# Optimization experiments

Hardware: AMD Instinct MI355X
Metric: run time of the kernel (lower is better)

The kernel has to match this reference:

```python
import jax, jax.numpy as jnp
import numpy as np

N_NODES = 100000
N_EDGES = 1600000
IN_DIM, HID, OUT = 64, 128, 128
NUM_GRAPHS = 64
BN_EPS = 1e-5


def setup_inputs() -> dict:
    key = jax.random.key(0)
    ks = jax.random.split(key, 16)
    x = jax.random.normal(ks[0], (N_NODES, IN_DIM), dtype=jnp.float32)
    edge_index = jax.random.randint(ks[1], (2, N_EDGES), 0, N_NODES, dtype=jnp.int32)
    batch = jnp.sort(jax.random.randint(ks[2], (N_NODES,), 0, NUM_GRAPHS, dtype=jnp.int32))
    dims = [IN_DIM, HID, HID, OUT]
    inp = {"x": x, "edge_index": edge_index, "batch": batch}
    for i in range(3):
        din, dout = dims[i], dims[i + 1]
        s = 1.0 / np.sqrt(din)
        inp[f"Ws{i}"] = jax.random.uniform(ks[3 + 4 * i], (din, dout), jnp.float32, -s, s)
        inp[f"Wi{i}"] = jax.random.uniform(ks[4 + 4 * i], (din, dout), jnp.float32, -s, s)
        inp[f"Wo{i}"] = jax.random.uniform(ks[5 + 4 * i], (din, dout), jnp.float32, -s, s)
        inp[f"g{i}"] = jnp.ones((dout,), jnp.float32)
        inp[f"b{i}"] = jnp.zeros((dout,), jnp.float32)
    return inp


def _dgcn(x, src, dst, Ws, Wi, Wo, gamma, beta):
    # directed aggregation: in-edges (messages from src land on dst) and out-edges
    agg_in = jax.ops.segment_sum(x[src], dst, num_segments=N_NODES)   # [N, d]
    agg_out = jax.ops.segment_sum(x[dst], src, num_segments=N_NODES)  # [N, d]
    out = x @ Ws + agg_in @ Wi + agg_out @ Wo
    out = jax.nn.relu(out)
    # BatchNorm1d (training mode, biased variance, as in torch)
    mu = out.mean(axis=0)
    var = ((out - mu) ** 2).mean(axis=0)
    return gamma * (out - mu) * jax.lax.rsqrt(var + BN_EPS) + beta


def reference(x, edge_index, batch, Ws0, Wi0, Wo0, g0, b0, Ws1, Wi1, Wo1, g1, b1,
              Ws2, Wi2, Wo2, g2, b2):
    src, dst = edge_index[0], edge_index[1]
    h = _dgcn(x, src, dst, Ws0, Wi0, Wo0, g0, b0)
    h = _dgcn(h, src, dst, Ws1, Wi1, Wo1, g1, b1)
    h = _dgcn(h, src, dst, Ws2, Wi2, Wo2, g2, b2)
    # global mean pool over graphs (dropout is identity at inference)
    sums = jax.ops.segment_sum(h, batch, num_segments=NUM_GRAPHS)       # [G, OUT]
    cnts = jax.ops.segment_sum(jnp.ones((N_NODES,), h.dtype), batch, num_segments=NUM_GRAPHS)
    return sums / jnp.maximum(cnts, 1.0)[:, None]
```

## Files before the change

kernel.cpp:

```cpp
#include <hip/hip_runtime.h>

#define NN 100000
#define NE 1600000
#define NG 64
#define BN_EPS 1e-5f

#define TOT (2 * NN)
#define STB 256

#define NB 98
#define BCAP 36864
#define EPB ((NE + 1023) / 1024)

typedef __attribute__((ext_vector_type(8))) short bf16x8;
typedef __attribute__((ext_vector_type(8))) unsigned short u16x8;
typedef __attribute__((ext_vector_type(4))) float f32x4;

__device__ __forceinline__ float bf2f(unsigned short u) {
  unsigned int i = (unsigned int)u << 16;
  float f; __builtin_memcpy(&f, &i, 4); return f;
}
__device__ __forceinline__ unsigned short f2bf(float f) {
  unsigned int i; __builtin_memcpy(&i, &f, 4);
  i += 0x7FFFu + ((i >> 16) & 1u);
  return (unsigned short)(i >> 16);
}

__device__ __forceinline__ int lower_bound_dev(const int* a, int n, int key) {
  int lo = 0, hi = n;
  while (lo < hi) { int mid = (lo + hi) >> 1; if (a[mid] < key) lo = mid + 1; else hi = mid; }
  return lo;
}

__global__ __launch_bounds__(256) void k_p1(const int* __restrict__ src,
    const int* __restrict__ dst, int* __restrict__ gcur, unsigned int* __restrict__ pairs) {
  __shared__ unsigned int lbuf[NB][64];
  __shared__ int lcnt[NB], lbase[NB];
  __shared__ int sc[256];
  int t = threadIdx.x;
  if (t < NB) lcnt[t] = 0;
  __syncthreads();
  int e0 = blockIdx.x * EPB;
  int e1 = min(e0 + EPB, NE);
  for (int e = e0 + t; e < e1; e += 256) {
    int s = src[e], d = dst[e];
    {
      int key = d;
      unsigned int val = ((unsigned int)(key & 2047) << 17) | (unsigned int)s;
      int bk = key >> 11;
      int p = atomicAdd(&lcnt[bk], 1);
      if (p < 64) lbuf[bk][p] = val;
      else { int g = atomicAdd(&gcur[bk], 1); pairs[(size_t)bk * BCAP + g] = val; }
    }
    {
      int key = s + NN;
      unsigned int val = ((unsigned int)(key & 2047) << 17) | (unsigned int)d;
      int bk = key >> 11;
      int p = atomicAdd(&lcnt[bk], 1);
      if (p < 64) lbuf[bk][p] = val;
      else { int g = atomicAdd(&gcur[bk], 1); pairs[(size_t)bk * BCAP + g] = val; }
    }
  }
  __syncthreads();
  if (t < NB) {
    int c = min(lcnt[t], 64);
    lcnt[t] = c;
    lbase[t] = atomicAdd(&gcur[t], c);
  }
  __syncthreads();
  sc[t] = (t < NB) ? lcnt[t] : 0;
  __syncthreads();
  for (int off = 1; off < 256; off <<= 1) {
    int x = (t >= off) ? sc[t - off] : 0;
    __syncthreads();
    sc[t] += x;
    __syncthreads();
  }
  int total = sc[NB - 1];
  for (int idx = t; idx < total; idx += 256) {
    int lo = 0, hi = NB - 1;
    while (lo < hi) { int mid = (lo + hi) >> 1; if (sc[mid] > idx) hi = mid; else lo = mid + 1; }
    int within = idx - ((lo == 0) ? 0 : sc[lo - 1]);
    pairs[(size_t)lo * BCAP + lbase[lo] + within] = lbuf[lo][within];
  }
}

__global__ void k_scan98(const int* __restrict__ gcur, int* __restrict__ fbase) {
  __shared__ int sc[128];
  int t = threadIdx.x;
  sc[t] = (t < NB) ? gcur[t] : 0;
  __syncthreads();
  for (int off = 1; off < 128; off <<= 1) {
    int x = (t >= off) ? sc[t - off] : 0;
    __syncthreads();
    sc[t] += x;
    __syncthreads();
  }
  if (t < NB) fbase[t] = (t == 0) ? 0 : sc[t - 1];
  if (t == 0) fbase[NB] = sc[NB - 1];
}

__global__ __launch_bounds__(256) void k_p2(const unsigned int* __restrict__ pairs,
    const int* __restrict__ gcur, const int* __restrict__ fbase,
    int* __restrict__ offs, int* __restrict__ nbr) {
  int b = blockIdx.x;
  int n = gcur[b];
  int base = fbase[b];
  __shared__ int hist[2048];
  __shared__ int sc[256];
  int t = threadIdx.x;
  #pragma unroll
  for (int j = 0; j < 8; ++j) hist[t * 8 + j] = 0;
  __syncthreads();
  const unsigned int* bp = pairs + (size_t)b * BCAP;
  for (int i = t; i < n; i += 256) atomicAdd(&hist[bp[i] >> 17], 1);
  __syncthreads();
  int v[8]; int tsum = 0;
  #pragma unroll
  for (int j = 0; j < 8; ++j) { v[j] = hist[t * 8 + j]; tsum += v[j]; }
  sc[t] = tsum;
  __syncthreads();
  for (int off = 1; off < 256; off <<= 1) {
    int x = (t >= off) ? sc[t - off] : 0;
    __syncthreads();
    sc[t] += x;
    __syncthreads();
  }
  int run = (t == 0) ? 0 : sc[t - 1];
  #pragma unroll
  for (int j = 0; j < 8; ++j) {
    int key = b * 2048 + t * 8 + j;
    if (key < TOT) offs[key] = base + run;
    hist[t * 8 + j] = run;
    run += v[j];
  }
  if (b == NB - 1 && t == 0) offs[TOT] = base + n;
  __syncthreads();
  for (int i = t; i < n; i += 256) {
    unsigned int u = bp[i];
    int lk = (int)(u >> 17);
    int pos = atomicAdd(&hist[lk], 1);
    nbr[base + pos] = (int)(u & 0x1FFFFu);
  }
}

__global__ __launch_bounds__(256) void k_cvt_x(const float* __restrict__ x,
                                               unsigned short* __restrict__ xb) {
  size_t i = (size_t)blockIdx.x * 256 + threadIdx.x;
  if (i >= (size_t)NN * 16) return;
  float4 v = *(const float4*)(x + i * 4);
  ushort4 o;
  o.x = f2bf(v.x); o.y = f2bf(v.y); o.z = f2bf(v.z); o.w = f2bf(v.w);
  *(ushort4*)(xb + i * 4) = o;
}

struct WtArgs { const float* W[9]; };
__global__ __launch_bounds__(256) void k_wt(WtArgs a, unsigned short* __restrict__ wt) {
  int t = blockIdx.x * 256 + threadIdx.x;
  if (t >= 15360) return;
  int p, rem, KS;
  if (t < 3072) { p = t >> 10; rem = t & 1023; KS = 2; }
  else { int u = t - 3072; p = 3 + (u >> 11); rem = u & 2047; KS = 4; }
  int ks = rem >> 9;
  int rem2 = rem & 511;
  int nt = rem2 >> 6;
  int lane = rem2 & 63;
  int L = p / 3, op = p - L * 3;
  int lbase = (L == 0) ? 0 : (24576 + (L - 1) * 49152);
  size_t dst = (size_t)lbase + (size_t)op * KS * 4096 + (size_t)(ks * 8 + nt) * 512 + lane * 8;
  const float* W = a.W[p];
  int krow = ks * 32 + (lane >> 4) * 8;
  int col = nt * 16 + (lane & 15);
  #pragma unroll
  for (int j = 0; j < 8; ++j)
    wt[dst + j] = f2bf(W[(size_t)(krow + j) * 128 + col]);
}

__global__ void k_ssid(float* __restrict__ ss) {
  int t = threadIdx.x;
  ss[t] = 1.f; ss[128 + t] = 0.f;
}

template<int DIN>
__global__ __launch_bounds__(256) void k_gather(const unsigned short* __restrict__ xb,
    const float* __restrict__ ss, const int* __restrict__ offs, const int* __restrict__ nbr,
    unsigned short* __restrict__ aggi, unsigned short* __restrict__ aggo) {
  constexpr int GW = DIN / 8;
  constexpr int GPB = 256 / GW;
  int g = blockIdx.x * GPB + threadIdx.x / GW;
  if (g >= TOT) return;
  int c0 = (threadIdx.x % GW) * 8;
  int beg = offs[g], end = offs[g + 1];
  float acc[8];
  #pragma unroll
  for (int j = 0; j < 8; ++j) acc[j] = 0.f;
  int k = beg;
  for (; k + 4 <= end; k += 4) {
    int n0 = nbr[k], n1 = nbr[k + 1], n2 = nbr[k + 2], n3 = nbr[k + 3];
    u16x8 v0 = *(const u16x8*)(xb + (size_t)n0 * DIN + c0);
    u16x8 v1 = *(const u16x8*)(xb + (size_t)n1 * DIN + c0);
    u16x8 v2 = *(const u16x8*)(xb + (size_t)n2 * DIN + c0);
    u16x8 v3 = *(const u16x8*)(xb + (size_t)n3 * DIN + c0);
    #pragma unroll
    for (int j = 0; j < 8; ++j)
      acc[j] += (bf2f(v0[j]) + bf2f(v1[j])) + (bf2f(v2[j]) + bf2f(v3[j]));
  }
  for (; k < end; ++k) {
    u16x8 v = *(const u16x8*)(xb + (size_t)nbr[k] * DIN + c0);
    #pragma unroll
    for (int j = 0; j < 8; ++j) acc[j] += bf2f(v[j]);
  }
  float cnt = (float)(end - beg);
  unsigned short r[8];
  #pragma unroll
  for (int j = 0; j < 8; ++j)
    r[j] = f2bf(fmaf(acc[j], ss[c0 + j], cnt * ss[128 + c0 + j]));
  unsigned short* o = (g < NN) ? (aggi + (size_t)g * DIN) : (aggo + (size_t)(g - NN) * DIN);
  *(u16x8*)(o + c0) = *(u16x8*)r;
}

template<int KD>
__global__ __launch_bounds__(256) void k_gemm(const unsigned short* __restrict__ A0,
    const float* __restrict__ ss, const unsigned short* __restrict__ A1,
    const unsigned short* __restrict__ A2, const unsigned short* __restrict__ wt,
    unsigned short* __restrict__ out) {
  constexpr int KS = KD / 32;
  int tid = threadIdx.x;
  int lane = tid & 63;
  int w = tid >> 6;
  int m0 = blockIdx.x * 64 + w * 16;
  int arow = m0 + (lane & 15);
  int koff = (lane >> 4) * 8;
  f32x4 acc[8];
  #pragma unroll
  for (int nt = 0; nt < 8; ++nt) acc[nt] = (f32x4){0.f, 0.f, 0.f, 0.f};

  const unsigned short* As[3] = {A0, A1, A2};
  #pragma unroll
  for (int op = 0; op < 3; ++op) {
    const unsigned short* __restrict__ A = As[op];
    bf16x8 af[KS];
    if (arow < NN) {
      #pragma unroll
      for (int ks = 0; ks < KS; ++ks)
        af[ks] = *(const bf16x8*)(A + (size_t)arow * KD + ks * 32 + koff);
      if (op == 0) {
        #pragma unroll
        for (int ks = 0; ks < KS; ++ks) {
          union { bf16x8 v; unsigned short u[8]; } tt;
          tt.v = af[ks];
          #pragma unroll
          for (int j = 0; j < 8; ++j) {
            int c = ks * 32 + koff + j;
            tt.u[j] = f2bf(fmaf(bf2f(tt.u[j]), ss[c], ss[128 + c]));
          }
          af[ks] = tt.v;
        }
      }
    } else {
      #pragma unroll
      for (int ks = 0; ks < KS; ++ks) af[ks] = (bf16x8){0,0,0,0,0,0,0,0};
    }
    #pragma unroll
    for (int ks = 0; ks < KS; ++ks) {
      #pragma unroll
      for (int nt = 0; nt < 8; ++nt) {
        bf16x8 bf = *(const bf16x8*)(wt + ((size_t)(op * KS + ks) * 8 + nt) * 512 + lane * 8);
        acc[nt] = __builtin_amdgcn_mfma_f32_16x16x32_bf16(af[ks], bf, acc[nt], 0, 0, 0);
      }
    }
  }

  __shared__ unsigned short lds[4][16][128];
  #pragma unroll
  for (int nt = 0; nt < 8; ++nt)
    #pragma unroll
    for (int r = 0; r < 4; ++r)
      lds[w][(lane >> 4) * 4 + r][nt * 16 + (lane & 15)] = f2bf(fmaxf(acc[nt][r], 0.f));
  #pragma unroll
  for (int it = 0; it < 4; ++it) {
    int rr = (lane >> 4) + it * 4;
    int cc = (lane & 15) * 8;
    int grow = m0 + rr;
    if (grow < NN)
      *(u16x8*)(out + (size_t)grow * 128 + cc) = *(const u16x8*)&lds[w][rr][cc];
  }
}

__global__ __launch_bounds__(256) void k_statsA(const unsigned short* __restrict__ hb,
                                                float* __restrict__ part) {
  int t = threadIdx.x;
  int q = t & 15;
  int gq = t >> 4;
  int c0 = q * 8;
  float s[8], s2[8];
  #pragma unroll
  for (int j = 0; j < 8; ++j) { s[j] = 0.f; s2[j] = 0.f; }
  for (int r = blockIdx.x * 16 + gq; r < NN; r += STB * 16) {
    u16x8 v = *(const u16x8*)(hb + (size_t)r * 128 + c0);
    #pragma unroll
    for (int j = 0; j < 8; ++j) {
      float f = bf2f(v[j]);
      s[j] += f;
      s2[j] = fmaf(f, f, s2[j]);
    }
  }
  __shared__ float ls[256][8], ls2[256][8];
  #pragma unroll
  for (int j = 0; j < 8; ++j) { ls[t][j] = s[j]; ls2[t][j] = s2[j]; }
  __syncthreads();
  if (t < 128) {
    int qq = t >> 3, jj = t & 7;
    float S = 0.f, S2 = 0.f;
    #pragma unroll
    for (int g = 0; g < 16; ++g) {
      S += ls[g * 16 + qq][jj];
      S2 += ls2[g * 16 + qq][jj];
    }
    part[(size_t)blockIdx.x * 256 + t] = S;
    part[(size_t)blockIdx.x * 256 + 128 + t] = S2;
  }
}

__global__ __launch_bounds__(256) void k_bn_final(const float* __restrict__ part,
    const float* __restrict__ g, const float* __restrict__ b, float* __restrict__ ss) {
  int t = threadIdx.x;
  float s = 0.f;
  for (int bb = 0; bb < STB; ++bb) s += part[(size_t)bb * 256 + t];
  __shared__ float tot[256];
  tot[t] = s; __syncthreads();
  if (t < 128) {
    float mu = tot[t] / (float)NN;
    float var = tot[128 + t] / (float)NN - mu * mu;
    float rs = rsqrtf(var + BN_EPS);
    float sc = rs * g[t];
    ss[t] = sc;
    ss[128 + t] = b[t] - mu * sc;
  }
}

__global__ __launch_bounds__(128) void k_pool(const unsigned short* __restrict__ hb,
    const int* __restrict__ batch, float* __restrict__ pool) {
  int c = threadIdx.x;
  int n0 = blockIdx.x * 256;
  if (n0 >= NN) return;
  int nend = n0 + 256; if (nend > NN) nend = NN;
  int cur = batch[n0];
  float run = 0.f;
  for (int n = n0; n < nend; ++n) {
    int g = batch[n];
    if (g != cur) { atomicAdd(&pool[(size_t)cur * 128 + c], run); run = 0.f; cur = g; }
    run += bf2f(hb[(size_t)n * 128 + c]);
  }
  atomicAdd(&pool[(size_t)cur * 128 + c], run);
}

__global__ __launch_bounds__(128) void k_final(const float* __restrict__ pool,
    const int* __restrict__ batch, const float* __restrict__ ss, float* __restrict__ out) {
  int g = blockIdx.x;
  int c = threadIdx.x;
  __shared__ int cnt;
  if (c == 0) {
    int lo = lower_bound_dev(batch, NN, g);
    int hi = lower_bound_dev(batch, NN, g + 1);
    cnt = hi - lo;
  }
  __syncthreads();
  float d = (float)(cnt > 1 ? cnt : 1);
  out[(size_t)g * 128 + c] = fmaf(pool[(size_t)g * 128 + c] / d, ss[c], ss[128 + c]);
}

extern "C" void kernel_launch(void* const* d_in, const int* in_sizes, int n_in,
                              void* d_out, int out_size, void* d_ws, size_t ws_size,
                              hipStream_t stream) {
  const float* x     = (const float*)d_in[0];
  const int*   ei    = (const int*)d_in[1];
  const int*   batch = (const int*)d_in[2];
  const float* gg[3] = {(const float*)d_in[6], (const float*)d_in[11], (const float*)d_in[16]};
  const float* bbv[3]= {(const float*)d_in[7], (const float*)d_in[12], (const float*)d_in[17]};
  const int* src = ei;
  const int* dst = ei + NE;

  uintptr_t p = ((uintptr_t)d_ws + 255) & ~(uintptr_t)255;
  auto alloc = [&](size_t bytes) { uintptr_t r = p; p = (p + bytes + 255) & ~(uintptr_t)255; return r; };

  unsigned int* pairs = (unsigned int*)alloc((size_t)NB * BCAP * 4);
  int* gcur  = (int*)alloc(NB * 4);
  int* fbase = (int*)alloc((NB + 1) * 4);
  int* offs  = (int*)alloc((TOT + 1) * 4);
  int* nbr   = (int*)alloc((size_t)2 * NE * 4);
  unsigned short* xb   = (unsigned short*)alloc((size_t)NN * 64 * 2);
  unsigned short* hb0  = (unsigned short*)alloc((size_t)NN * 128 * 2);
  unsigned short* hb1  = (unsigned short*)alloc((size_t)NN * 128 * 2);
  unsigned short* hb2  = (unsigned short*)alloc((size_t)NN * 128 * 2);
  unsigned short* aggi = (unsigned short*)alloc((size_t)NN * 128 * 2);
  unsigned short* aggo = (unsigned short*)alloc((size_t)NN * 128 * 2);
  unsigned short* wt   = (unsigned short*)alloc(122880 * 2);
  float* part  = (float*)alloc((size_t)STB * 256 * 4);
  float* ss_id = (float*)alloc(256 * 4);
  float* ss0   = (float*)alloc(256 * 4);
  float* ss1   = (float*)alloc(256 * 4);
  float* ss2   = (float*)alloc(256 * 4);
  float* pool  = (float*)alloc((size_t)NG * 128 * 4);

  const int gemm_grid = (NN + 63) / 64;

  hipMemsetAsync(gcur, 0, NB * sizeof(int), stream);
  k_p1<<<1024, 256, 0, stream>>>(src, dst, gcur, pairs);
  k_scan98<<<1, 128, 0, stream>>>(gcur, fbase);
  k_p2<<<NB, 256, 0, stream>>>(pairs, gcur, fbase, offs, nbr);

  k_cvt_x<<<(NN * 16 + 255) / 256, 256, 0, stream>>>(x, xb);
  WtArgs wa;
  wa.W[0] = (const float*)d_in[3];  wa.W[1] = (const float*)d_in[4];  wa.W[2] = (const float*)d_in[5];
  wa.W[3] = (const float*)d_in[8];  wa.W[4] = (const float*)d_in[9];  wa.W[5] = (const float*)d_in[10];
  wa.W[6] = (const float*)d_in[13]; wa.W[7] = (const float*)d_in[14]; wa.W[8] = (const float*)d_in[15];
  k_wt<<<60, 256, 0, stream>>>(wa, wt);
  k_ssid<<<1, 128, 0, stream>>>(ss_id);

  k_gather<64><<<(TOT + 31) / 32, 256, 0, stream>>>(xb, ss_id, offs, nbr, aggi, aggo);
  k_gemm<64><<<gemm_grid, 256, 0, stream>>>(xb, ss_id, aggi, aggo, wt + 0, hb0);
  k_statsA<<<STB, 256, 0, stream>>>(hb0, part);
  k_bn_final<<<1, 256, 0, stream>>>(part, gg[0], bbv[0], ss0);

  k_gather<128><<<(TOT + 15) / 16, 256, 0, stream>>>(hb0, ss0, offs, nbr, aggi, aggo);
  k_gemm<128><<<gemm_grid, 256, 0, stream>>>(hb0, ss0, aggi, aggo, wt + 24576, hb1);
  k_statsA<<<STB, 256, 0, stream>>>(hb1, part);
  k_bn_final<<<1, 256, 0, stream>>>(part, gg[1], bbv[1], ss1);

  k_gather<128><<<(TOT + 15) / 16, 256, 0, stream>>>(hb1, ss1, offs, nbr, aggi, aggo);
  k_gemm<128><<<gemm_grid, 256, 0, stream>>>(hb1, ss1, aggi, aggo, wt + 73728, hb2);
  k_statsA<<<STB, 256, 0, stream>>>(hb2, part);
  k_bn_final<<<1, 256, 0, stream>>>(part, gg[2], bbv[2], ss2);

  hipMemsetAsync(pool, 0, (size_t)NG * 128 * 4, stream);
  k_pool<<<(NN + 255) / 256, 128, 0, stream>>>(hb2, batch, pool);
  k_final<<<NG, 128, 0, stream>>>(pool, batch, ss2, (float*)d_out);
}
```

Baseline: 626.1 us.

## Switch storage from bf16 to fp16 with packed half gather and sorted neighbor writes

All intermediate activations and weights are now stored as fp16 instead of bf16. The gather accumulates neighbour rows with packed half-precision vector adds, and the GEMM uses the f16 MFMA intrinsic. Separately, the CSR fill pass now scatters neighbours in eight passes grouped by node-id range, which gives the neighbour lists a partial sort that should improve gather locality. Accumulating in fp16 cuts conversion ALU work but risks precision loss or overflow on high-degree sums, and the multi-pass scatter rereads the bucket eight times.

```diff
diff --git a/kernel.cpp b/kernel.cpp
--- a/kernel.cpp
+++ b/kernel.cpp
@@ -12,18 +12,15 @@
 #define BCAP 36864
 #define EPB ((NE + 1023) / 1024)
 
-typedef __attribute__((ext_vector_type(8))) short bf16x8;
+typedef __attribute__((ext_vector_type(8))) _Float16 f16x8;
 typedef __attribute__((ext_vector_type(8))) unsigned short u16x8;
 typedef __attribute__((ext_vector_type(4))) float f32x4;
 
-__device__ __forceinline__ float bf2f(unsigned short u) {
-  unsigned int i = (unsigned int)u << 16;
-  float f; __builtin_memcpy(&f, &i, 4); return f;
-}
-__device__ __forceinline__ unsigned short f2bf(float f) {
-  unsigned int i; __builtin_memcpy(&i, &f, 4);
-  i += 0x7FFFu + ((i >> 16) & 1u);
-  return (unsigned short)(i >> 16);
+__device__ __forceinline__ float h2f(unsigned short u) {
+  _Float16 h; __builtin_memcpy(&h, &u, 2); return (float)h;
+}
+__device__ __forceinline__ unsigned short f2h(float f) {
+  _Float16 h = (_Float16)f; unsigned short u; __builtin_memcpy(&u, &h, 2); return u;
 }
 
 __device__ __forceinline__ int lower_bound_dev(const int* a, int n, int key) {
@@ -136,11 +133,17 @@
   }
   if (b == NB - 1 && t == 0) offs[TOT] = base + n;
   __syncthreads();
-  for (int i = t; i < n; i += 256) {
-    unsigned int u = bp[i];
-    int lk = (int)(u >> 17);
-    int pos = atomicAdd(&hist[lk], 1);
-    nbr[base + pos] = (int)(u & 0x1FFFFu);
+  for (int q = 0; q < 8; ++q) {
+    for (int i = t; i < n; i += 256) {
+      unsigned int u = bp[i];
+      unsigned int pay = u & 0x1FFFFu;
+      if ((int)(pay >> 14) == q) {
+        int lk = (int)(u >> 17);
+        int pos = atomicAdd(&hist[lk], 1);
+        nbr[base + pos] = (int)pay;
+      }
+    }
+    __syncthreads();
   }
 }
 
@@ -150,7 +153,7 @@
   if (i >= (size_t)NN * 16) return;
   float4 v = *(const float4*)(x + i * 4);
   ushort4 o;
-  o.x = f2bf(v.x); o.y = f2bf(v.y); o.z = f2bf(v.z); o.w = f2bf(v.w);
+  o.x = f2h(v.x); o.y = f2h(v.y); o.z = f2h(v.z); o.w = f2h(v.w);
   *(ushort4*)(xb + i * 4) = o;
 }
 
@@ -173,7 +176,7 @@
   int col = nt * 16 + (lane & 15);
   #pragma unroll
   for (int j = 0; j < 8; ++j)
-    wt[dst + j] = f2bf(W[(size_t)(krow + j) * 128 + col]);
+    wt[dst + j] = f2h(W[(size_t)(krow + j) * 128 + col]);
 }
 
 __global__ void k_ssid(float* __restrict__ ss) {
@@ -191,30 +194,27 @@
   if (g >= TOT) return;
   int c0 = (threadIdx.x % GW) * 8;
   int beg = offs[g], end = offs[g + 1];
-  float acc[8];
-  #pragma unroll
-  for (int j = 0; j < 8; ++j) acc[j] = 0.f;
+  f16x8 acc;
+  #pragma unroll
+  for (int j = 0; j < 8; ++j) acc[j] = (_Float16)0.f;
   int k = beg;
   for (; k + 4 <= end; k += 4) {
     int n0 = nbr[k], n1 = nbr[k + 1], n2 = nbr[k + 2], n3 = nbr[k + 3];
-    u16x8 v0 = *(const u16x8*)(xb + (size_t)n0 * DIN + c0);
-    u16x8 v1 = *(const u16x8*)(xb + (size_t)n1 * DIN + c0);
-    u16x8 v2 = *(const u16x8*)(xb + (size_t)n2 * DIN + c0);
-    u16x8 v3 = *(const u16x8*)(xb + (size_t)n3 * DIN + c0);
-    #pragma unroll
-    for (int j = 0; j < 8; ++j)
-      acc[j] += (bf2f(v0[j]) + bf2f(v1[j])) + (bf2f(v2[j]) + bf2f(v3[j]));
+    f16x8 v0 = *(const f16x8*)(xb + (size_t)n0 * DIN + c0);
+    f16x8 v1 = *(const f16x8*)(xb + (size_t)n1 * DIN + c0);
+    f16x8 v2 = *(const f16x8*)(xb + (size_t)n2 * DIN + c0);
+    f16x8 v3 = *(const f16x8*)(xb + (size_t)n3 * DIN + c0);
+    acc += (v0 + v1) + (v2 + v3);
   }
   for (; k < end; ++k) {
-    u16x8 v = *(const u16x8*)(xb + (size_t)nbr[k] * DIN + c0);
-    #pragma unroll
-    for (int j = 0; j < 8; ++j) acc[j] += bf2f(v[j]);
+    f16x8 v = *(const f16x8*)(xb + (size_t)nbr[k] * DIN + c0);
+    acc += v;
   }
   float cnt = (float)(end - beg);
   unsigned short r[8];
   #pragma unroll
   for (int j = 0; j < 8; ++j)
-    r[j] = f2bf(fmaf(acc[j], ss[c0 + j], cnt * ss[128 + c0 + j]));
+    r[j] = f2h(fmaf((float)acc[j], ss[c0 + j], cnt * ss[128 + c0 + j]));
   unsigned short* o = (g < NN) ? (aggi + (size_t)g * DIN) : (aggo + (size_t)(g - NN) * DIN);
   *(u16x8*)(o + c0) = *(u16x8*)r;
 }
@@ -239,34 +239,33 @@
   #pragma unroll
   for (int op = 0; op < 3; ++op) {
     const unsigned short* __restrict__ A = As[op];
-    bf16x8 af[KS];
+    f16x8 af[KS];
     if (arow < NN) {
       #pragma unroll
       for (int ks = 0; ks < KS; ++ks)
-        af[ks] = *(const bf16x8*)(A + (size_t)arow * KD + ks * 32 + koff);
+        af[ks] = *(const f16x8*)(A + (size_t)arow * KD + ks * 32 + koff);
       if (op == 0) {
         #pragma unroll
         for (int ks = 0; ks < KS; ++ks) {
-          union { bf16x8 v; unsigned short u[8]; } tt;
-          tt.v = af[ks];
           #pragma unroll
           for (int j = 0; j < 8; ++j) {
             int c = ks * 32 + koff + j;
-            tt.u[j] = f2bf(fmaf(bf2f(tt.u[j]), ss[c], ss[128 + c]));
+            af[ks][j] = (_Float16)fmaf((float)af[ks][j], ss[c], ss[128 + c]);
           }
-          af[ks] = tt.v;
         }
       }
     } else {
       #pragma unroll
-      for (int ks = 0; ks < KS; ++ks) af[ks] = (bf16x8){0,0,0,0,0,0,0,0};
+      for (int ks = 0; ks < KS; ++ks)
+        #pragma unroll
+        for (int j = 0; j < 8; ++j) af[ks][j] = (_Float16)0.f;
     }
     #pragma unroll
     for (int ks = 0; ks < KS; ++ks) {
       #pragma unroll
       for (int nt = 0; nt < 8; ++nt) {
-        bf16x8 bf = *(const bf16x8*)(wt + ((size_t)(op * KS + ks) * 8 + nt) * 512 + lane * 8);
-        acc[nt] = __builtin_amdgcn_mfma_f32_16x16x32_bf16(af[ks], bf, acc[nt], 0, 0, 0);
+        f16x8 bf = *(const f16x8*)(wt + ((size_t)(op * KS + ks) * 8 + nt) * 512 + lane * 8);
+        acc[nt] = __builtin_amdgcn_mfma_f32_16x16x32_f16(af[ks], bf, acc[nt], 0, 0, 0);
       }
     }
   }
@@ -276,7 +275,7 @@
   for (int nt = 0; nt < 8; ++nt)
     #pragma unroll
     for (int r = 0; r < 4; ++r)
-      lds[w][(lane >> 4) * 4 + r][nt * 16 + (lane & 15)] = f2bf(fmaxf(acc[nt][r], 0.f));
+      lds[w][(lane >> 4) * 4 + r][nt * 16 + (lane & 15)] = f2h(fmaxf(acc[nt][r], 0.f));
   #pragma unroll
   for (int it = 0; it < 4; ++it) {
     int rr = (lane >> 4) + it * 4;
@@ -300,7 +299,7 @@
     u16x8 v = *(const u16x8*)(hb + (size_t)r * 128 + c0);
     #pragma unroll
     for (int j = 0; j < 8; ++j) {
-      float f = bf2f(v[j]);
+      float f = h2f(v[j]);
       s[j] += f;
       s2[j] = fmaf(f, f, s2[j]);
     }
@@ -350,7 +349,7 @@
   for (int n = n0; n < nend; ++n) {
     int g = batch[n];
     if (g != cur) { atomicAdd(&pool[(size_t)cur * 128 + c], run); run = 0.f; cur = g; }
-    run += bf2f(hb[(size_t)n * 128 + c]);
+    run += h2f(hb[(size_t)n * 128 + c]);
   }
   atomicAdd(&pool[(size_t)cur * 128 + c], run);
 }
```

New measurement: 810.9 us. 29.5% more time.
